# Performance work log

Hardware: AMD Instinct MI355X
Metric: run time of the kernel (lower is better)

Reference implementation:

```python
import jax, jax.numpy as jnp
import numpy as np


def setup_inputs() -> dict:
    key = jax.random.key(0)
    k1, k2, k3, k4 = jax.random.split(key, 4)
    B, L, H, E = 2, 10000, 8, 64
    NE = 160000
    return {
        "queries": jax.random.normal(k1, (B, L, H, E), dtype=jnp.float32),
        "keys": jax.random.normal(k2, (B, L, H, E), dtype=jnp.float32),
        "values": jax.random.normal(k3, (B, L, H, E), dtype=jnp.float32),
        "adj": jax.random.randint(k4, (2, NE), 0, L, dtype=jnp.int64),
    }


def reference(queries, keys, values, adj):
    # queries/keys/values: [B, L, H, E]; adj: [2, NE] (row 0 = dst group, row 1 = src)
    B, L, H, E = queries.shape
    softmax_temp = 1.0 / (E ** 0.5)
    dst = adj[0]
    src = adj[1]

    # edge-gather dot product: qk[b, e, h] = sum_d q[b, dst[e], h, d] * k[b, src[e], h, d]
    qk = jnp.sum(queries[:, dst] * keys[:, src], axis=-1) * softmax_temp  # [B, NE, H]

    # segment softmax grouped by destination node (dropout is identity at eval)
    qk_e = qk.transpose(1, 0, 2)  # [NE, B, H] (segment ops act on leading axis)
    seg_max = jax.ops.segment_max(qk_e, dst, num_segments=L)  # [L, B, H]
    ex = jnp.exp(qk_e - seg_max[dst])
    seg_sum = jax.ops.segment_sum(ex, dst, num_segments=L)  # [L, B, H]
    alpha = ex / (seg_sum[dst] + 1e-16)  # [NE, B, H]

    # spmm: gather v at src, weight by alpha, scatter-add to dst
    weighted = values[:, src] * alpha.transpose(1, 0, 2)[..., None]  # [B, NE, H, E]
    out = jnp.zeros_like(values).at[:, dst].add(weighted)  # [B, L, H, E]
    return out
```

## Files before the change

kernel.cpp:

```cpp
#include <hip/hip_runtime.h>

#define BB 2
#define HH 8
#define EE 64
#define ROW (HH * EE)
#define HC 4

typedef float vf4 __attribute__((ext_vector_type(4)));

__device__ inline unsigned short f2bf(float f) {
  unsigned int u = __float_as_uint(f);
  u = (u + 0x7fffu + ((u >> 16) & 1u)) >> 16;
  return (unsigned short)u;
}

__global__ __launch_bounds__(256) void convert_hist_kernel(
    const float* __restrict__ k, const float* __restrict__ v,
    unsigned short* __restrict__ kbf, unsigned short* __restrict__ vbf,
    const int* __restrict__ dst, int* __restrict__ counts,
    int n4, int NE) {
  int i = blockIdx.x * blockDim.x + threadIdx.x;
  if (i < n4) {
    vf4 kf = __builtin_nontemporal_load((const vf4*)k + i);
    vf4 vf = __builtin_nontemporal_load((const vf4*)v + i);
    ((ushort4*)kbf)[i] = make_ushort4(f2bf(kf.x), f2bf(kf.y), f2bf(kf.z), f2bf(kf.w));
    ((ushort4*)vbf)[i] = make_ushort4(f2bf(vf.x), f2bf(vf.y), f2bf(vf.z), f2bf(vf.w));
  }
  if (i < NE) {
    atomicAdd(&counts[dst[i]], 1);
  }
}

__global__ __launch_bounds__(1024) void scan_kernel(
    const int* __restrict__ counts_in, int* __restrict__ counts_mut,
    int* __restrict__ offsets, int L) {
  __shared__ int sums[1024];
  int tid = threadIdx.x;
  int chunk = (L + 1023) / 1024;
  int beg = tid * chunk;
  int end = min(beg + chunk, L);
  int s = 0;
  for (int i = beg; i < end; ++i) s += counts_in[i];
  sums[tid] = s;
  __syncthreads();
  for (int off = 1; off < 1024; off <<= 1) {
    int val = 0;
    if (tid >= off) val = sums[tid - off];
    __syncthreads();
    if (tid >= off) sums[tid] += val;
    __syncthreads();
  }
  int run = (tid > 0) ? sums[tid - 1] : 0;
  for (int i = beg; i < end; ++i) {
    offsets[i] = run;
    run += counts_in[i];
    counts_mut[i] = 0;
  }
  if (tid == 1023) offsets[L] = run;
}

__global__ __launch_bounds__(256) void fill_csr_kernel(
    const int* __restrict__ dst, const int* __restrict__ src,
    const int* __restrict__ offsets, int* __restrict__ cursor,
    int* __restrict__ csr_src, int NE) {
  int e = blockIdx.x * blockDim.x + threadIdx.x;
  if (e >= NE) return;
  int d = dst[e];
  int pos = atomicAdd(&cursor[d], 1);
  csr_src[offsets[d] + pos] = src[e];
}

__device__ inline void bf8_unpack(uint4 u, float* f) {
  f[0] = __uint_as_float(u.x << 16);
  f[1] = __uint_as_float(u.x & 0xffff0000u);
  f[2] = __uint_as_float(u.y << 16);
  f[3] = __uint_as_float(u.y & 0xffff0000u);
  f[4] = __uint_as_float(u.z << 16);
  f[5] = __uint_as_float(u.z & 0xffff0000u);
  f[6] = __uint_as_float(u.w << 16);
  f[7] = __uint_as_float(u.w & 0xffff0000u);
}

__global__ __launch_bounds__(256) void fused_attn_kernel(
    const float* __restrict__ q, const unsigned short* __restrict__ kbf,
    const unsigned short* __restrict__ vbf, const int* __restrict__ offsets,
    const int* __restrict__ csr_src, float* __restrict__ out, int L) {
  const int lane = threadIdx.x & 63;
  const int wslot = blockIdx.x * (blockDim.x >> 6) + (threadIdx.x >> 6);
  const int wstride = gridDim.x * (blockDim.x >> 6);
  const int nwid = L * BB;

  for (int wid = wslot; wid < nwid; wid += wstride) {
    int d = wid >> 1;
    int b = wid & 1;
    int beg = offsets[d];
    int end = offsets[d + 1];

    const vf4* qrow = (const vf4*)(q + ((size_t)b * L + d) * ROW);
    vf4 q0 = __builtin_nontemporal_load(qrow + lane * 2 + 0);
    vf4 q1 = __builtin_nontemporal_load(qrow + lane * 2 + 1);
    q0 *= 0.125f;
    q1 *= 0.125f;

    float m = -INFINITY;
    float l_run = 0.0f;
    float acc[8];
#pragma unroll
    for (int i = 0; i < 8; ++i) acc[i] = 0.0f;

    const uint4* kb_base = (const uint4*)(kbf + (size_t)b * L * ROW);
    const uint4* vb_base = (const uint4*)(vbf + (size_t)b * L * ROW);

    for (int t0 = beg; t0 < end; t0 += 2 * HC) {
      int cnt = min(2 * HC, end - t0);
      uint4 kk[2 * HC], vv[2 * HC];
#pragma unroll
      for (int i = 0; i < 2 * HC; ++i) {
        if (i < cnt) {
          unsigned s = (unsigned)csr_src[t0 + i];
          kk[i] = kb_base[s * (unsigned)(ROW / 8) + lane];
          vv[i] = vb_base[s * (unsigned)(ROW / 8) + lane];
        }
      }
      float qk[2 * HC];
      float cmax = -INFINITY;
#pragma unroll
      for (int i = 0; i < 2 * HC; ++i) {
        qk[i] = -INFINITY;
        if (i < cnt) {
          float kf[8];
          bf8_unpack(kk[i], kf);
          float p = q0.x * kf[0] + q0.y * kf[1] + q0.z * kf[2] + q0.w * kf[3] +
                    q1.x * kf[4] + q1.y * kf[5] + q1.z * kf[6] + q1.w * kf[7];
          p += __shfl_xor(p, 1);
          p += __shfl_xor(p, 2);
          p += __shfl_xor(p, 4);
          qk[i] = p;
          cmax = fmaxf(cmax, p);
        }
      }
      if (__any(cmax > m)) {
        float mnew = fmaxf(m, cmax);
        float scale = __expf(m - mnew);
        l_run *= scale;
#pragma unroll
        for (int i = 0; i < 8; ++i) acc[i] *= scale;
        m = mnew;
      }
#pragma unroll
      for (int i = 0; i < 2 * HC; ++i) {
        if (i < cnt) {
          float a = __expf(qk[i] - m);
          l_run += a;
          float vf[8];
          bf8_unpack(vv[i], vf);
#pragma unroll
          for (int j = 0; j < 8; ++j) acc[j] += a * vf[j];
        }
      }
    }

    float r = 1.0f / (l_run + 1e-16f);
    vf4* orow = (vf4*)(out + ((size_t)b * L + d) * ROW);
    vf4 o0 = {acc[0] * r, acc[1] * r, acc[2] * r, acc[3] * r};
    vf4 o1 = {acc[4] * r, acc[5] * r, acc[6] * r, acc[7] * r};
    __builtin_nontemporal_store(o0, orow + lane * 2 + 0);
    __builtin_nontemporal_store(o1, orow + lane * 2 + 1);
  }
}

extern "C" void kernel_launch(void* const* d_in, const int* in_sizes, int n_in,
                              void* d_out, int out_size, void* d_ws, size_t ws_size,
                              hipStream_t stream) {
  const float* q = (const float*)d_in[0];
  const float* k = (const float*)d_in[1];
  const float* v = (const float*)d_in[2];
  const int* adj = (const int*)d_in[3];

  const int NE = in_sizes[3] / 2;
  const int L = in_sizes[0] / (BB * HH * EE);
  const int* dst = adj;
  const int* src = adj + NE;
  const int nelem = BB * L * HH * EE;

  char* ws = (char*)d_ws;
  size_t off = 0;
  unsigned short* kbf = (unsigned short*)(ws + off); off += (size_t)nelem * 2;
  unsigned short* vbf = (unsigned short*)(ws + off); off += (size_t)nelem * 2;
  int* counts = (int*)(ws + off);   off += (size_t)L * 4;
  int* offsets = (int*)(ws + off);  off += (size_t)(L + 1) * 4;
  int* csr_src = (int*)(ws + off);  off += (size_t)NE * 4;

  hipMemsetAsync(counts, 0, (size_t)L * 4, stream);

  int n4 = nelem / 4;
  convert_hist_kernel<<<(n4 + 255) / 256, 256, 0, stream>>>(
      k, v, kbf, vbf, dst, counts, n4, NE);

  scan_kernel<<<1, 1024, 0, stream>>>(counts, counts, offsets, L);

  fill_csr_kernel<<<(NE + 255) / 256, 256, 0, stream>>>(
      dst, src, offsets, counts, csr_src, NE);

  int nwaves = L * BB;
  int nblocks = min(2048, (nwaves + 3) / 4);
  fused_attn_kernel<<<nblocks, 256, 0, stream>>>(
      q, kbf, vbf, offsets, csr_src, (float*)d_out, L);
}
```

Before: 292.1 us.

## Interleave K/V rows and double-buffer edge gathers via async global-to-LDS loads

```diff
diff --git a/kernel.cpp b/kernel.cpp
--- a/kernel.cpp
+++ b/kernel.cpp
@@ -4,7 +4,8 @@
 #define HH 8
 #define EE 64
 #define ROW (HH * EE)
-#define HC 4
+#define KVROW 2048
+#define CH 2
 
 typedef float vf4 __attribute__((ext_vector_type(4)));
 
@@ -16,15 +17,19 @@
 
 __global__ __launch_bounds__(256) void convert_hist_kernel(
     const float* __restrict__ k, const float* __restrict__ v,
-    unsigned short* __restrict__ kbf, unsigned short* __restrict__ vbf,
+    unsigned short* __restrict__ kv,
     const int* __restrict__ dst, int* __restrict__ counts,
     int n4, int NE) {
   int i = blockIdx.x * blockDim.x + threadIdx.x;
   if (i < n4) {
     vf4 kf = __builtin_nontemporal_load((const vf4*)k + i);
     vf4 vf = __builtin_nontemporal_load((const vf4*)v + i);
-    ((ushort4*)kbf)[i] = make_ushort4(f2bf(kf.x), f2bf(kf.y), f2bf(kf.z), f2bf(kf.w));
-    ((ushort4*)vbf)[i] = make_ushort4(f2bf(vf.x), f2bf(vf.y), f2bf(vf.z), f2bf(vf.w));
+    int row = i >> 7;
+    int off4 = i & 127;
+    ((ushort4*)kv)[row * 256 + off4] =
+        make_ushort4(f2bf(kf.x), f2bf(kf.y), f2bf(kf.z), f2bf(kf.w));
+    ((ushort4*)kv)[row * 256 + 128 + off4] =
+        make_ushort4(f2bf(vf.x), f2bf(vf.y), f2bf(vf.z), f2bf(vf.w));
   }
   if (i < NE) {
     atomicAdd(&counts[dst[i]], 1);
@@ -81,12 +86,34 @@
   f[7] = __uint_as_float(u.w & 0xffff0000u);
 }
 
+#define ISSUE_CHUNK(BUF, T0)                                               \
+  {                                                                        \
+    _Pragma("unroll") for (int i_ = 0; i_ < CH; ++i_) {                    \
+      int e_ = (T0) + i_;                                                  \
+      unsigned s_ = (e_ < end) ? (unsigned)csr_src[e_] : 0u;               \
+      const char* row_ = kv_base + s_ * (unsigned)KVROW + lane * 16u;      \
+      __builtin_amdgcn_global_load_lds(                                    \
+          (const __attribute__((address_space(1))) unsigned int*)row_,     \
+          (__attribute__((address_space(3))) unsigned int*)((BUF) + i_ * KVROW), \
+          16, 0, 0);                                                       \
+      __builtin_amdgcn_global_load_lds(                                    \
+          (const __attribute__((address_space(1))) unsigned int*)(row_ + 1024), \
+          (__attribute__((address_space(3))) unsigned int*)((BUF) + i_ * KVROW + 1024), \
+          16, 0, 0);                                                       \
+    }                                                                      \
+  }
+
 __global__ __launch_bounds__(256) void fused_attn_kernel(
-    const float* __restrict__ q, const unsigned short* __restrict__ kbf,
-    const unsigned short* __restrict__ vbf, const int* __restrict__ offsets,
-    const int* __restrict__ csr_src, float* __restrict__ out, int L) {
+    const float* __restrict__ q, const unsigned short* __restrict__ kv,
+    const int* __restrict__ offsets, const int* __restrict__ csr_src,
+    float* __restrict__ out, int L) {
+  __shared__ __align__(16) char smem[4][2][CH * KVROW];
   const int lane = threadIdx.x & 63;
-  const int wslot = blockIdx.x * (blockDim.x >> 6) + (threadIdx.x >> 6);
+  const int warp = threadIdx.x >> 6;
+  char* buf0 = &smem[warp][0][0];
+  char* buf1 = &smem[warp][1][0];
+
+  const int wslot = blockIdx.x * (blockDim.x >> 6) + warp;
   const int wstride = gridDim.x * (blockDim.x >> 6);
   const int nwid = L * BB;
 
@@ -97,10 +124,24 @@
     int end = offsets[d + 1];
 
     const vf4* qrow = (const vf4*)(q + ((size_t)b * L + d) * ROW);
+    vf4* orow = (vf4*)(out + ((size_t)b * L + d) * ROW);
+
+    if (beg >= end) {
+      vf4 z = {0.f, 0.f, 0.f, 0.f};
+      __builtin_nontemporal_store(z, orow + lane * 2 + 0);
+      __builtin_nontemporal_store(z, orow + lane * 2 + 1);
+      continue;
+    }
+
+    const char* kv_base = (const char*)kv + (size_t)b * L * KVROW;
+
+    ISSUE_CHUNK(buf0, beg);
+
     vf4 q0 = __builtin_nontemporal_load(qrow + lane * 2 + 0);
     vf4 q1 = __builtin_nontemporal_load(qrow + lane * 2 + 1);
-    q0 *= 0.125f;
-    q1 *= 0.125f;
+    const float qscale = 0.125f * 1.44269504f;
+    q0 *= qscale;
+    q1 *= qscale;
 
     float m = -INFINITY;
     float l_run = 0.0f;
@@ -108,65 +149,58 @@
 #pragma unroll
     for (int i = 0; i < 8; ++i) acc[i] = 0.0f;
 
-    const uint4* kb_base = (const uint4*)(kbf + (size_t)b * L * ROW);
-    const uint4* vb_base = (const uint4*)(vbf + (size_t)b * L * ROW);
-
-    for (int t0 = beg; t0 < end; t0 += 2 * HC) {
-      int cnt = min(2 * HC, end - t0);
-      uint4 kk[2 * HC], vv[2 * HC];
-#pragma unroll
-      for (int i = 0; i < 2 * HC; ++i) {
-        if (i < cnt) {
-          unsigned s = (unsigned)csr_src[t0 + i];
-          kk[i] = kb_base[s * (unsigned)(ROW / 8) + lane];
-          vv[i] = vb_base[s * (unsigned)(ROW / 8) + lane];
-        }
-      }
-      float qk[2 * HC];
+    int nch = (end - beg + CH - 1) / CH;
+    for (int c = 0; c < nch; ++c) {
+      char* cur = (c & 1) ? buf1 : buf0;
+      char* nxt = (c & 1) ? buf0 : buf1;
+      int t0 = beg + c * CH;
+      ISSUE_CHUNK(nxt, t0 + CH);
+      asm volatile("s_waitcnt vmcnt(4)" ::: "memory");
+      __builtin_amdgcn_sched_barrier(0);
+
+      float qk[CH];
       float cmax = -INFINITY;
 #pragma unroll
-      for (int i = 0; i < 2 * HC; ++i) {
-        qk[i] = -INFINITY;
-        if (i < cnt) {
-          float kf[8];
-          bf8_unpack(kk[i], kf);
-          float p = q0.x * kf[0] + q0.y * kf[1] + q0.z * kf[2] + q0.w * kf[3] +
-                    q1.x * kf[4] + q1.y * kf[5] + q1.z * kf[6] + q1.w * kf[7];
-          p += __shfl_xor(p, 1);
-          p += __shfl_xor(p, 2);
-          p += __shfl_xor(p, 4);
-          qk[i] = p;
-          cmax = fmaxf(cmax, p);
-        }
+      for (int i = 0; i < CH; ++i) {
+        uint4 kk = *(const uint4*)(cur + i * KVROW + lane * 16);
+        float kf[8];
+        bf8_unpack(kk, kf);
+        float p = q0.x * kf[0] + q0.y * kf[1] + q0.z * kf[2] + q0.w * kf[3] +
+                  q1.x * kf[4] + q1.y * kf[5] + q1.z * kf[6] + q1.w * kf[7];
+        p += __shfl_xor(p, 1);
+        p += __shfl_xor(p, 2);
+        p += __shfl_xor(p, 4);
+        p = (t0 + i < end) ? p : -INFINITY;
+        qk[i] = p;
+        cmax = fmaxf(cmax, p);
       }
       if (__any(cmax > m)) {
         float mnew = fmaxf(m, cmax);
-        float scale = __expf(m - mnew);
+        float scale = exp2f(m - mnew);
         l_run *= scale;
 #pragma unroll
         for (int i = 0; i < 8; ++i) acc[i] *= scale;
         m = mnew;
       }
 #pragma unroll
-      for (int i = 0; i < 2 * HC; ++i) {
-        if (i < cnt) {
-          float a = __expf(qk[i] - m);
-          l_run += a;
-          float vf[8];
-          bf8_unpack(vv[i], vf);
-#pragma unroll
-          for (int j = 0; j < 8; ++j) acc[j] += a * vf[j];
-        }
+      for (int i = 0; i < CH; ++i) {
+        float a = exp2f(qk[i] - m);
+        l_run += a;
+        uint4 vv = *(const uint4*)(cur + i * KVROW + 1024 + lane * 16);
+        float vf[8];
+        bf8_unpack(vv, vf);
+#pragma unroll
+        for (int j = 0; j < 8; ++j) acc[j] += a * vf[j];
       }
     }
 
     float r = 1.0f / (l_run + 1e-16f);
-    vf4* orow = (vf4*)(out + ((size_t)b * L + d) * ROW);
     vf4 o0 = {acc[0] * r, acc[1] * r, acc[2] * r, acc[3] * r};
     vf4 o1 = {acc[4] * r, acc[5] * r, acc[6] * r, acc[7] * r};
     __builtin_nontemporal_store(o0, orow + lane * 2 + 0);
     __builtin_nontemporal_store(o1, orow + lane * 2 + 1);
   }
+  asm volatile("s_waitcnt vmcnt(0)" ::: "memory");
 }
 
 extern "C" void kernel_launch(void* const* d_in, const int* in_sizes, int n_in,
@@ -185,8 +219,7 @@
 
   char* ws = (char*)d_ws;
   size_t off = 0;
-  unsigned short* kbf = (unsigned short*)(ws + off); off += (size_t)nelem * 2;
-  unsigned short* vbf = (unsigned short*)(ws + off); off += (size_t)nelem * 2;
+  unsigned short* kv = (unsigned short*)(ws + off); off += (size_t)nelem * 4;
   int* counts = (int*)(ws + off);   off += (size_t)L * 4;
   int* offsets = (int*)(ws + off);  off += (size_t)(L + 1) * 4;
   int* csr_src = (int*)(ws + off);  off += (size_t)NE * 4;
@@ -195,7 +228,7 @@
 
   int n4 = nelem / 4;
   convert_hist_kernel<<<(n4 + 255) / 256, 256, 0, stream>>>(
-      k, v, kbf, vbf, dst, counts, n4, NE);
+      k, v, kv, dst, counts, n4, NE);
 
   scan_kernel<<<1, 1024, 0, stream>>>(counts, counts, offsets, L);
 
@@ -203,7 +236,7 @@
       dst, src, offsets, counts, csr_src, NE);
 
   int nwaves = L * BB;
-  int nblocks = min(2048, (nwaves + 3) / 4);
+  int nblocks = min(1280, (nwaves + 3) / 4);
   fused_attn_kernel<<<nblocks, 256, 0, stream>>>(
-      q, kbf, vbf, offsets, csr_src, (float*)d_out, L);
-}
+      q, kv, offsets, csr_src, (float*)d_out, L);
+}
```

Result: slower. 310.3 us (+6.2%).
